# Kernel tuning notes

Hardware: AMD Instinct MI355X
Metric: run time of the kernel (lower is better)

The kernel has to match this reference:

```python
import jax, jax.numpy as jnp
import numpy as np

EMBED = 1024
HEADS = 16
HEAD_DIM = EMBED // HEADS
NEG = -1e20


def setup_inputs() -> dict:
    key = jax.random.key(0)
    ks = jax.random.split(key, 12)
    N, S, E = 2, 2048, EMBED
    w = lambda k: (jax.random.normal(k, (E, E), dtype=jnp.float32) * 0.02)
    b = lambda k: (jax.random.normal(k, (E,), dtype=jnp.float32) * 0.02)
    return {
        "values": jax.random.normal(ks[0], (N, S, E), dtype=jnp.float32),
        "keys": jax.random.normal(ks[1], (N, S, E), dtype=jnp.float32),
        "query": jax.random.normal(ks[2], (N, S, E), dtype=jnp.float32),
        "mask": jnp.ones((N, S), dtype=jnp.int32),
        "Wv": w(ks[3]), "bv": b(ks[4]),
        "Wk": w(ks[5]), "bk": b(ks[6]),
        "Wq": w(ks[7]), "bq": b(ks[8]),
        "Wo": w(ks[9]), "bo": b(ks[10]),
    }


def reference(values, keys, query, mask, Wv, bv, Wk, bk, Wq, bq, Wo, bo):
    N, S, E = query.shape
    # torch nn.Linear: x @ W.T + b
    v = (values @ Wv.T + bv).reshape(N, S, HEADS, HEAD_DIM)
    k = (keys @ Wk.T + bk).reshape(N, S, HEADS, HEAD_DIM)
    q = (query @ Wq.T + bq).reshape(N, S, HEADS, HEAD_DIM)
    # full [N,H,Q,K] score matrix, as in the original einsum
    energy = jnp.einsum('nqhd,nkhd->nhqk', q, k)
    # 2D mask with mismatched dims triggers causal tril path in the original
    causal = jnp.tril(jnp.ones((S, S), dtype=bool))  # [Q,K]
    energy = jnp.where(causal[None, None, :, :], energy, NEG)
    # NOTE: original scales by sqrt(embed_size), not sqrt(head_dim)
    attn = jax.nn.softmax(energy / jnp.sqrt(jnp.float32(E)), axis=3)
    out = jnp.einsum('nhqk,nkhd->nqhd', attn, v).reshape(N, S, E)
    return out @ Wo.T + bo
```

## Files before the change

### kernel.cpp

```cpp
#include <hip/hip_runtime.h>

typedef __bf16 bf16;
typedef __bf16 bf16x4 __attribute__((ext_vector_type(4)));
typedef __bf16 bf16x8 __attribute__((ext_vector_type(8)));
typedef float floatx4 __attribute__((ext_vector_type(4)));

#define GLOAD_LDS16(gp, lp) \
  __builtin_amdgcn_global_load_lds( \
      (const __attribute__((address_space(1))) void*)(gp), \
      (__attribute__((address_space(3))) void*)(lp), 16, 0, 0)

__global__ __launch_bounds__(256) void cvt_all_kernel(
    const float* __restrict__ v, const float* __restrict__ k, const float* __restrict__ q,
    const float* __restrict__ wv, const float* __restrict__ wk,
    const float* __restrict__ wq, const float* __restrict__ wo,
    bf16* __restrict__ xv, bf16* __restrict__ xk, bf16* __restrict__ xq,
    bf16* __restrict__ bwv, bf16* __restrict__ bwk, bf16* __restrict__ bwq,
    bf16* __restrict__ bwo) {
  const int i = blockIdx.x * 256 + threadIdx.x;
  const int A4 = 1 << 20;
  const float* src; bf16* dst; int off;
  if (i < A4)            { src = v; dst = xv; off = i; }
  else if (i < 2 * A4)   { src = k; dst = xk; off = i - A4; }
  else if (i < 3 * A4)   { src = q; dst = xq; off = i - 2 * A4; }
  else {
    int j = i - 3 * A4; int r = j >> 18; off = j & ((1 << 18) - 1);
    src = (r == 0) ? wv : (r == 1) ? wk : (r == 2) ? wq : wo;
    dst = (r == 0) ? bwv : (r == 1) ? bwk : (r == 2) ? bwq : bwo;
  }
  float4 x = reinterpret_cast<const float4*>(src)[off];
  union { bf16 b[4]; short4 s; } u;
  u.b[0] = (bf16)x.x; u.b[1] = (bf16)x.y; u.b[2] = (bf16)x.z; u.b[3] = (bf16)x.w;
  reinterpret_cast<short4*>(dst)[off] = u.s;
}

template <int MODE>
__device__ __forceinline__ void gemm_body(
    const bf16* __restrict__ A, const bf16* __restrict__ B,
    const float* __restrict__ bias, void* __restrict__ Cout) {
  constexpr int K = 1024, N = 1024;
  __shared__ __align__(16) bf16 SMEM[8192];
  bf16* As = SMEM;
  bf16* Bs = SMEM + 4096;
  const int tid = threadIdx.x;
  const int lane = tid & 63;
  const int wave = tid >> 6;
  const int quad = lane >> 4;
  const int l16 = lane & 15;
  const int wm = (wave >> 1) * 64;
  const int wn = (wave & 1) * 64;
  const int am0 = blockIdx.y * 128;
  const int bn0 = blockIdx.x * 128;
  const int srow = lane >> 2;
  const int scol = (lane & 3) * 8;

  floatx4 acc[4][4] = {};

  for (int k0 = 0; k0 < K; k0 += 32) {
    __syncthreads();
#pragma unroll
    for (int j = 0; j < 2; j++) {
      const int chunk = wave * 2 + j;
      const int row = chunk * 16 + srow;
      GLOAD_LDS16(A + (size_t)(am0 + row) * K + k0 + scol, As + chunk * 512);
      GLOAD_LDS16(B + (size_t)(bn0 + row) * K + k0 + scol, Bs + chunk * 512);
    }
    __syncthreads();

    bf16x8 af[4], bfv[4];
#pragma unroll
    for (int mi = 0; mi < 4; mi++)
      af[mi] = *reinterpret_cast<const bf16x8*>(&As[(wm + mi * 16 + l16) * 32 + quad * 8]);
#pragma unroll
    for (int ni = 0; ni < 4; ni++)
      bfv[ni] = *reinterpret_cast<const bf16x8*>(&Bs[(wn + ni * 16 + l16) * 32 + quad * 8]);
#pragma unroll
    for (int mi = 0; mi < 4; mi++)
#pragma unroll
      for (int ni = 0; ni < 4; ni++)
        acc[mi][ni] = __builtin_amdgcn_mfma_f32_16x16x32_bf16(af[mi], bfv[ni], acc[mi][ni], 0, 0, 0);
  }

  if constexpr (MODE == 2) {
#pragma unroll
    for (int mi = 0; mi < 4; mi++) {
#pragma unroll
      for (int ni = 0; ni < 4; ni++) {
        const int col = bn0 + wn + ni * 16 + l16;
        const float bb = bias[col];
        const int row = am0 + wm + mi * 16 + quad * 4;
#pragma unroll
        for (int r = 0; r < 4; r++)
          reinterpret_cast<float*>(Cout)[(size_t)(row + r) * N + col] = acc[mi][ni][r] + bb;
      }
    }
  } else {
    __syncthreads();
    bf16* T = SMEM + wave * 2048;
    const int nb = (am0 + wm) >> 11;
    const int sq0 = (am0 + wm) & 2047;
    const int h = (bn0 + wn) >> 6;
    const int nh = nb * 16 + h;
    const int r8 = lane >> 3, c8 = lane & 7;

    if constexpr (MODE == 0) {
#pragma unroll
      for (int pp = 0; pp < 2; pp++) {
#pragma unroll
        for (int mm = 0; mm < 2; mm++) {
          const int mi = pp * 2 + mm;
#pragma unroll
          for (int ni = 0; ni < 4; ni++) {
            const int d = ni * 16 + l16;
            const float bc = bias[bn0 + wn + d];
#pragma unroll
            for (int r = 0; r < 4; r++) {
              const int s = mm * 16 + quad * 4 + r;
              T[s * 64 + (d & 7) + 8 * ((d >> 3) ^ (s & 7))] = (bf16)(acc[mi][ni][r] + bc);
            }
          }
        }
#pragma unroll
        for (int it = 0; it < 4; it++) {
          const int s = it * 8 + r8;
          bf16x8 vv = *reinterpret_cast<const bf16x8*>(&T[s * 64 + ((c8 ^ r8) * 8)]);
          *reinterpret_cast<bf16x8*>(
              reinterpret_cast<bf16*>(Cout) +
              ((size_t)nh * 2048 + sq0 + pp * 32 + s) * 64 + c8 * 8) = vv;
        }
      }
    } else {
#pragma unroll
      for (int pp = 0; pp < 2; pp++) {
#pragma unroll
        for (int nn = 0; nn < 2; nn++) {
          const int ni = pp * 2 + nn;
          const int dp = nn * 16 + l16;
          const float bc = bias[bn0 + wn + pp * 32 + dp];
#pragma unroll
          for (int mi = 0; mi < 4; mi++) {
#pragma unroll
            for (int r = 0; r < 4; r++) {
              const int s = mi * 16 + quad * 4 + r;
              T[dp * 64 + (s & 7) + 8 * ((s >> 3) ^ (dp & 7))] = (bf16)(acc[mi][ni][r] + bc);
            }
          }
        }
#pragma unroll
        for (int it = 0; it < 4; it++) {
          const int dp = it * 8 + r8;
          bf16x8 vv = *reinterpret_cast<const bf16x8*>(&T[dp * 64 + ((c8 ^ r8) * 8)]);
          *reinterpret_cast<bf16x8*>(
              reinterpret_cast<bf16*>(Cout) +
              ((size_t)nh * 64 + pp * 32 + dp) * 2048 + sq0 + c8 * 8) = vv;
        }
      }
    }
  }
}

__global__ __launch_bounds__(256) void gemm_qkv(
    const bf16* __restrict__ A0, const bf16* __restrict__ B0, const float* __restrict__ c0, bf16* __restrict__ C0,
    const bf16* __restrict__ A1, const bf16* __restrict__ B1, const float* __restrict__ c1, bf16* __restrict__ C1,
    const bf16* __restrict__ A2, const bf16* __restrict__ B2, const float* __restrict__ c2, bf16* __restrict__ C2) {
  if (blockIdx.z == 0)      gemm_body<0>(A0, B0, c0, C0);
  else if (blockIdx.z == 1) gemm_body<0>(A1, B1, c1, C1);
  else                      gemm_body<1>(A2, B2, c2, C2);
}

__global__ __launch_bounds__(256) void gemm_out(
    const bf16* __restrict__ A, const bf16* __restrict__ B,
    const float* __restrict__ bias, float* __restrict__ C) {
  gemm_body<2>(A, B, bias, C);
}

#define S_LEN 2048
#define EMB 1024
#define QT 128
#define KTILE 64
#define PSTR 72
#define SCALE2 (0.03125f * 1.44269504f)

__global__ __launch_bounds__(256) void attn_kernel(
    const bf16* __restrict__ Qh, const bf16* __restrict__ Kh,
    const bf16* __restrict__ Vt, bf16* __restrict__ O,
    float* __restrict__ Opart, float* __restrict__ lpart) {
  __shared__ __align__(16) bf16 Ks[2 * KTILE * 64];
  __shared__ __align__(16) bf16 Vs[2 * 64 * KTILE];
  __shared__ __align__(16) bf16 Ps[QT * PSTR];

  const int tid = threadIdx.x;
  const int lane = tid & 63;
  const int wave = tid >> 6;
  const int quad = lane >> 4;
  const int l16 = lane & 15;
  const int wq = wave * 32;

  const int c = blockIdx.x;
  const int role = blockIdx.y;
  const int nh = c >> 3;
  const int t = c & 7;
  const int n = nh >> 4;
  const int h = nh & 15;
  int qt, kt0, kt1;
  if (role == 0) { qt = t; kt0 = 0; kt1 = 2 * t + 2; }
  else {
    qt = 15 - t;
    const int halfk = qt + 1;
    kt0 = (role == 1) ? 0 : halfk;
    kt1 = (role == 1) ? halfk : 2 * halfk;
  }
  const int q0 = qt * QT;

  bf16x8 aq[2][2];
  {
    const bf16* Qb = Qh + ((size_t)nh * S_LEN + q0 + wq + l16) * 64 + quad * 8;
#pragma unroll
    for (int mi = 0; mi < 2; mi++)
#pragma unroll
      for (int kc = 0; kc < 2; kc++)
        aq[mi][kc] = *reinterpret_cast<const bf16x8*>(Qb + mi * 16 * 64 + kc * 32);
  }

  float l_part[2] = {};
  floatx4 o_acc[2][4] = {};

  const bf16* Kbase = Kh + (size_t)nh * S_LEN * 64;
  const bf16* Vbase = Vt + (size_t)nh * 64 * S_LEN;

  const int srl = lane >> 3;
  const int sc8 = lane & 7;

  auto stage = [&](int kt) {
    const int k0s = kt * KTILE;
    const int buf = (kt & 1) * 4096;
#pragma unroll
    for (int j = 0; j < 2; j++) {
      const int rl = wave * 16 + j * 8 + srl;
      const int c8s = ((sc8 ^ (rl & 7)) * 8);
      GLOAD_LDS16(Kbase + (size_t)(k0s + rl) * 64 + c8s, Ks + buf + (wave * 16 + j * 8) * 64);
      GLOAD_LDS16(Vbase + (size_t)rl * S_LEN + k0s + c8s, Vs + buf + (wave * 16 + j * 8) * 64);
    }
  };

  stage(kt0);
  for (int kt = kt0; kt < kt1; kt++) {
    const int k0 = kt * KTILE;
    __syncthreads();
    if (kt + 1 < kt1) stage(kt + 1);
    const bf16* Kc = Ks + (kt & 1) * 4096;
    const bf16* Vc = Vs + (kt & 1) * 4096;

    floatx4 s_acc[2][4] = {};
#pragma unroll
    for (int kc = 0; kc < 2; kc++) {
      bf16x8 bk[4];
#pragma unroll
      for (int ni = 0; ni < 4; ni++)
        bk[ni] = *reinterpret_cast<const bf16x8*>(
            &Kc[(ni * 16 + l16) * 64 + (((kc * 4 + quad) ^ (l16 & 7)) * 8)]);
#pragma unroll
      for (int mi = 0; mi < 2; mi++)
#pragma unroll
        for (int ni = 0; ni < 4; ni++)
          s_acc[mi][ni] = __builtin_amdgcn_mfma_f32_16x16x32_bf16(bk[ni], aq[mi][kc], s_acc[mi][ni], 0, 0, 0);
    }

    const bool needMask = (k0 + KTILE - 1) > (q0 + wq);
    const int qg = q0 + wq + l16;
#pragma unroll
    for (int mi = 0; mi < 2; mi++) {
#pragma unroll
      for (int ni = 0; ni < 4; ni++) {
        const int kgb = k0 + ni * 16 + quad * 4;
        bf16x4 pk;
#pragma unroll
        for (int r = 0; r < 4; r++) {
          float pr = __builtin_amdgcn_exp2f(s_acc[mi][ni][r] * SCALE2);
          if (needMask) pr = ((kgb + r) <= (qg + mi * 16)) ? pr : 0.f;
          l_part[mi] += pr;
          pk[r] = (bf16)pr;
        }
        *reinterpret_cast<bf16x4*>(
            &Ps[(wq + mi * 16 + l16) * PSTR + ni * 16 + quad * 4]) = pk;
      }
    }

#pragma unroll
    for (int kc = 0; kc < 2; kc++) {
      bf16x8 ap[2], bv[4];
#pragma unroll
      for (int mi = 0; mi < 2; mi++)
        ap[mi] = *reinterpret_cast<const bf16x8*>(
            &Ps[(wq + mi * 16 + l16) * PSTR + kc * 32 + quad * 8]);
#pragma unroll
      for (int di = 0; di < 4; di++)
        bv[di] = *reinterpret_cast<const bf16x8*>(
            &Vc[(di * 16 + l16) * 64 + (((kc * 4 + quad) ^ (l16 & 7)) * 8)]);
#pragma unroll
      for (int mi = 0; mi < 2; mi++)
#pragma unroll
        for (int di = 0; di < 4; di++)
          o_acc[mi][di] = __builtin_amdgcn_mfma_f32_16x16x32_bf16(ap[mi], bv[di], o_acc[mi][di], 0, 0, 0);
    }
  }

  float l_sum[2];
#pragma unroll
  for (int mi = 0; mi < 2; mi++) {
    float s = l_part[mi];
    s += __shfl_xor(s, 16);
    s += __shfl_xor(s, 32);
    l_sum[mi] = s;
  }

  if (role == 0) {
    bf16* Op = O + ((size_t)(n * S_LEN + q0 + wq)) * EMB + h * 64;
#pragma unroll
    for (int mi = 0; mi < 2; mi++) {
      const float linv = 1.0f / l_sum[mi];
#pragma unroll
      for (int r = 0; r < 4; r++) {
        const float inv = __shfl(linv, quad * 4 + r);
        bf16* orow = Op + (size_t)(mi * 16 + quad * 4 + r) * EMB;
#pragma unroll
        for (int di = 0; di < 4; di++)
          orow[di * 16 + l16] = (bf16)(o_acc[mi][di][r] * inv);
      }
    }
  } else {
    float* Ob = Opart + ((size_t)c * 2 + (role - 1)) * (QT * 64);
    float* lb = lpart + ((size_t)c * 2 + (role - 1)) * QT;
#pragma unroll
    for (int mi = 0; mi < 2; mi++)
      if (lane < 16) lb[wq + mi * 16 + lane] = l_sum[mi];
#pragma unroll
    for (int mi = 0; mi < 2; mi++)
#pragma unroll
      for (int r = 0; r < 4; r++) {
        float* orow = Ob + (size_t)(wq + mi * 16 + quad * 4 + r) * 64;
#pragma unroll
        for (int di = 0; di < 4; di++)
          orow[di * 16 + l16] = o_acc[mi][di][r];
      }
  }
}

__global__ __launch_bounds__(256) void attn_combine(
    const float* __restrict__ Opart, const float* __restrict__ lpart,
    bf16* __restrict__ O) {
  const int c = blockIdx.x;
  const int nh = c >> 3;
  const int t = c & 7;
  const int qt = 15 - t;
  const int n = nh >> 4;
  const int h = nh & 15;
  const float* O1 = Opart + (size_t)c * 2 * (QT * 64);
  const float* O2 = O1 + QT * 64;
  const float* l1 = lpart + (size_t)c * 2 * QT;
  const float* l2 = l1 + QT;
  const int tid = threadIdx.x;
  for (int i = tid; i < QT * 64 / 4; i += 256) {
    const int row = i >> 4;
    const float inv = 1.0f / (l1[row] + l2[row]);
    float4 a = reinterpret_cast<const float4*>(O1)[i];
    float4 b = reinterpret_cast<const float4*>(O2)[i];
    bf16x4 pk;
    pk[0] = (bf16)((a.x + b.x) * inv);
    pk[1] = (bf16)((a.y + b.y) * inv);
    pk[2] = (bf16)((a.z + b.z) * inv);
    pk[3] = (bf16)((a.w + b.w) * inv);
    *reinterpret_cast<bf16x4*>(
        O + ((size_t)(n * S_LEN + qt * QT + row)) * EMB + h * 64 + (i & 15) * 4) = pk;
  }
}

extern "C" void kernel_launch(void* const* d_in, const int* in_sizes, int n_in,
                              void* d_out, int out_size, void* d_ws, size_t ws_size,
                              hipStream_t stream) {
  (void)in_sizes; (void)n_in; (void)out_size; (void)ws_size;
  const float* values = (const float*)d_in[0];
  const float* keys   = (const float*)d_in[1];
  const float* query  = (const float*)d_in[2];
  const float* Wv = (const float*)d_in[4];
  const float* bv = (const float*)d_in[5];
  const float* Wk = (const float*)d_in[6];
  const float* bk = (const float*)d_in[7];
  const float* Wq = (const float*)d_in[8];
  const float* bq = (const float*)d_in[9];
  const float* Wo = (const float*)d_in[10];
  const float* bo = (const float*)d_in[11];
  float* out = (float*)d_out;

  const int NB = 2, S = 2048, E = 1024;
  const int M = NB * S;
  const size_t MB_ = 1u << 20;
  char* ws = (char*)d_ws;
  bf16* xv  = (bf16*)(ws + 0 * MB_);
  bf16* xk  = (bf16*)(ws + 8 * MB_);
  bf16* xq  = (bf16*)(ws + 16 * MB_);
  bf16* wvb = (bf16*)(ws + 24 * MB_);
  bf16* wkb = (bf16*)(ws + 26 * MB_);
  bf16* wqb = (bf16*)(ws + 28 * MB_);
  bf16* wob = (bf16*)(ws + 30 * MB_);
  bf16* kh  = (bf16*)(ws + 32 * MB_);
  bf16* qh  = (bf16*)(ws + 40 * MB_);
  bf16* vt  = (bf16*)(ws + 48 * MB_);
  bf16* ao  = (bf16*)(ws + 56 * MB_);
  float* Opart = (float*)(ws + 0 * MB_);
  float* lpart = (float*)(ws + 17 * MB_);

  cvt_all_kernel<<<(4 << 20) / 256, 256, 0, stream>>>(
      values, keys, query, Wv, Wk, Wq, Wo,
      xv, xk, xq, wvb, wkb, wqb, wob);

  gemm_qkv<<<dim3(E / 128, M / 128, 3), 256, 0, stream>>>(
      xq, wqb, bq, qh,
      xk, wkb, bk, kh,
      xv, wvb, bv, vt);

  attn_kernel<<<dim3(256, 3), 256, 0, stream>>>(qh, kh, vt, ao, Opart, lpart);
  attn_combine<<<dim3(256), 256, 0, stream>>>(Opart, lpart, ao);

  gemm_out<<<dim3(E / 128, M / 128), 256, 0, stream>>>(ao, wob, bo, out);
}
```

Baseline: 235.0 us.

## Double-buffer A tiles in LDS and load B fragments directly into registers

Result: slower. 257.0 us (+9.3%).

```diff
diff --git a/kernel.cpp b/kernel.cpp
--- a/kernel.cpp
+++ b/kernel.cpp
@@ -39,9 +39,8 @@
     const bf16* __restrict__ A, const bf16* __restrict__ B,
     const float* __restrict__ bias, void* __restrict__ Cout) {
   constexpr int K = 1024, N = 1024;
+  constexpr int NSTEP = K / 32;
   __shared__ __align__(16) bf16 SMEM[8192];
-  bf16* As = SMEM;
-  bf16* Bs = SMEM + 4096;
   const int tid = threadIdx.x;
   const int lane = tid & 63;
   const int wave = tid >> 6;
@@ -56,29 +55,48 @@
 
   floatx4 acc[4][4] = {};
 
-  for (int k0 = 0; k0 < K; k0 += 32) {
-    __syncthreads();
+  auto stageA = [&](int step, int bufsel) {
+    const int k0 = step * 32;
+    bf16* As = SMEM + bufsel * 4096;
 #pragma unroll
     for (int j = 0; j < 2; j++) {
       const int chunk = wave * 2 + j;
       const int row = chunk * 16 + srow;
       GLOAD_LDS16(A + (size_t)(am0 + row) * K + k0 + scol, As + chunk * 512);
-      GLOAD_LDS16(B + (size_t)(bn0 + row) * K + k0 + scol, Bs + chunk * 512);
-    }
-    __syncthreads();
-
-    bf16x8 af[4], bfv[4];
+    }
+  };
+
+  auto loadB = [&](bf16x8 (&bb)[4], int step) {
+    const int k0 = step * 32;
+#pragma unroll
+    for (int ni = 0; ni < 4; ni++)
+      bb[ni] = *reinterpret_cast<const bf16x8*>(
+          B + (size_t)(bn0 + wn + ni * 16 + l16) * K + k0 + quad * 8);
+  };
+
+  auto compute = [&](const bf16* As, const bf16x8 (&bb)[4]) {
+    bf16x8 af[4];
 #pragma unroll
     for (int mi = 0; mi < 4; mi++)
       af[mi] = *reinterpret_cast<const bf16x8*>(&As[(wm + mi * 16 + l16) * 32 + quad * 8]);
 #pragma unroll
-    for (int ni = 0; ni < 4; ni++)
-      bfv[ni] = *reinterpret_cast<const bf16x8*>(&Bs[(wn + ni * 16 + l16) * 32 + quad * 8]);
-#pragma unroll
     for (int mi = 0; mi < 4; mi++)
 #pragma unroll
       for (int ni = 0; ni < 4; ni++)
-        acc[mi][ni] = __builtin_amdgcn_mfma_f32_16x16x32_bf16(af[mi], bfv[ni], acc[mi][ni], 0, 0, 0);
+        acc[mi][ni] = __builtin_amdgcn_mfma_f32_16x16x32_bf16(af[mi], bb[ni], acc[mi][ni], 0, 0, 0);
+  };
+
+  bf16x8 bA[4], bB[4];
+  stageA(0, 0);
+  loadB(bA, 0);
+  for (int t = 0; t < NSTEP; t += 2) {
+    __syncthreads();
+    stageA(t + 1, 1);
+    loadB(bB, t + 1);
+    compute(SMEM, bA);
+    __syncthreads();
+    if (t + 2 < NSTEP) { stageA(t + 2, 0); loadB(bA, t + 2); }
+    compute(SMEM + 4096, bB);
   }
 
   if constexpr (MODE == 2) {
@@ -159,7 +177,7 @@
   }
 }
 
-__global__ __launch_bounds__(256) void gemm_qkv(
+__global__ __launch_bounds__(256, 3) void gemm_qkv(
     const bf16* __restrict__ A0, const bf16* __restrict__ B0, const float* __restrict__ c0, bf16* __restrict__ C0,
     const bf16* __restrict__ A1, const bf16* __restrict__ B1, const float* __restrict__ c1, bf16* __restrict__ C1,
     const bf16* __restrict__ A2, const bf16* __restrict__ B2, const float* __restrict__ c2, bf16* __restrict__ C2) {
@@ -168,7 +186,7 @@
   else                      gemm_body<1>(A2, B2, c2, C2);
 }
 
-__global__ __launch_bounds__(256) void gemm_out(
+__global__ __launch_bounds__(256, 3) void gemm_out(
     const bf16* __restrict__ A, const bf16* __restrict__ B,
     const float* __restrict__ bias, float* __restrict__ C) {
   gemm_body<2>(A, B, bias, C);
```
